# Kernel tuning notes

Measured on AMD Instinct MI355X. Metric: run time of the kernel, lower is better.

## Reference

```python
import jax, jax.numpy as jnp
import numpy as np

N, E = 50000, 800000
D_IN_N, D_IN_E, D_OUT = 64, 64, 64


def setup_inputs() -> dict:
    key = jax.random.key(0)
    ks = jax.random.split(key, 10)
    stdv = 1.0 / np.sqrt(D_OUT)
    u = lambda k, shape: jax.random.uniform(k, shape, jnp.float32, -stdv, stdv)
    return {
        "nf": jax.random.normal(ks[0], (N, D_IN_N), jnp.float32),
        "ef": jax.random.normal(ks[1], (E, D_IN_E), jnp.float32),
        "src": jax.random.randint(ks[2], (E,), 0, N, jnp.int32),
        "dst": jax.random.randint(ks[3], (E,), 0, N, jnp.int32),
        "W_node": u(ks[4], (D_IN_N, D_OUT)),
        "W_edge": u(ks[5], (D_IN_E, D_OUT)),
        "bias_node": u(ks[6], (D_OUT,)),
        "bias_edge": u(ks[7], (D_OUT,)),
        "W_dense": u(ks[8], (2 * D_OUT, D_OUT)),  # Linear(2*out, out) weight, stored transposed
        "b_dense": u(ks[9], (D_OUT,)),
    }


def reference(nf, ef, src, dst, W_node, W_edge, bias_node, bias_edge, W_dense, b_dense):
    n_nodes = nf.shape[0]
    # input projections
    nf_h = nf @ W_node                     # [N, D]
    ef_h = ef @ W_edge                     # [E, D]
    # update_all: mean of incoming edge features per dst node (0 for isolated nodes, DGL default)
    deg = jax.ops.segment_sum(jnp.ones((ef_h.shape[0],), ef_h.dtype), dst, num_segments=n_nodes)
    nb_ef = jax.ops.segment_sum(ef_h, dst, num_segments=n_nodes) / jnp.maximum(deg, 1.0)[:, None]
    # apply_nodes: nf = act(nf + bias)
    nf_out = jax.nn.relu(nf_h + bias_node)
    # apply_edges (uses updated nf): cat([ef + nb_ef[dst], (nf[src]+nf[dst])/2]) -> Linear -> +bias -> act
    tmp_ef = ef_h + nb_ef[dst]             # [E, D]
    srcdst_nf = (nf_out[src] + nf_out[dst]) * 0.5
    ef_out = jnp.concatenate([tmp_ef, srcdst_nf], axis=1) @ W_dense + b_dense + bias_edge
    ef_out = jax.nn.relu(ef_out)
    return nf_out, ef_out
```

## Files before the change

### kernel.cpp

```cpp
#include <hip/hip_runtime.h>

#define D 64

typedef __attribute__((ext_vector_type(8))) short short8;
typedef __attribute__((ext_vector_type(4))) float f32x4;

__device__ __forceinline__ ushort f2b(float f) {
    union { float f; unsigned u; } x; x.f = f;
    unsigned r = x.u + 0x7FFFu + ((x.u >> 16) & 1u);
    return (ushort)(r >> 16);
}
__device__ __forceinline__ float b2f(ushort u) {
    union { float f; unsigned u; } x; x.u = ((unsigned)u) << 16;
    return x.f;
}
__device__ __forceinline__ short8 pack8(float4 a, float4 b) {
    short8 r;
    r[0] = (short)f2b(a.x); r[1] = (short)f2b(a.y); r[2] = (short)f2b(a.z); r[3] = (short)f2b(a.w);
    r[4] = (short)f2b(b.x); r[5] = (short)f2b(b.y); r[6] = (short)f2b(b.z); r[7] = (short)f2b(b.w);
    return r;
}

#define LDA 72

__global__ __launch_bounds__(256) void fused_front_kernel(
    const float* __restrict__ nf, const float* __restrict__ Wn,
    const float* __restrict__ bias, const float* __restrict__ Wd,
    float* __restrict__ out, ushort* __restrict__ nfp_b, int N,
    const int* __restrict__ dst, int* __restrict__ deg_i, int E,
    const float* __restrict__ W_edge, const float* __restrict__ b_dense,
    const float* __restrict__ bias_edge, ushort* __restrict__ Wcomb_b,
    float* __restrict__ bias2, int NPB, int HB)
{
    __shared__ ushort Bn[64 * LDA];
    __shared__ ushort Bd[64 * LDA];
    __shared__ ushort Vs[64 * LDA];
    const int tid = threadIdx.x;
    const int bid = blockIdx.x;

    if (bid < NPB) {
        const long row0 = (long)bid * 64;
        const int w = tid >> 6, lane = tid & 63;
        const int lr = lane & 15, g = lane >> 4;
        const bool odd = lane & 1;

        {
            int k = tid >> 2, n0 = (tid & 3) * 16;
            const float4* wr = (const float4*)(Wn + (long)k * D + n0);
            float4 v0 = wr[0], v1 = wr[1], v2 = wr[2], v3 = wr[3];
            float vs[16] = {v0.x, v0.y, v0.z, v0.w, v1.x, v1.y, v1.z, v1.w,
                            v2.x, v2.y, v2.z, v2.w, v3.x, v3.y, v3.z, v3.w};
            #pragma unroll
            for (int j = 0; j < 16; ++j) Bn[(n0 + j) * LDA + k] = f2b(vs[j]);
            const float4* wd = (const float4*)(Wd + (long)(D + k) * D + n0);
            float4 u0 = wd[0], u1 = wd[1], u2 = wd[2], u3 = wd[3];
            float us[16] = {u0.x, u0.y, u0.z, u0.w, u1.x, u1.y, u1.z, u1.w,
                            u2.x, u2.y, u2.z, u2.w, u3.x, u3.y, u3.z, u3.w};
            #pragma unroll
            for (int j = 0; j < 16; ++j) Bd[(n0 + j) * LDA + k] = f2b(0.5f * us[j]);
        }

        long era = row0 + 16 * w + lr; if (era >= N) era = N - 1;
        const float4* ap = (const float4*)(nf + era * D);
        float4 v0 = ap[2 * g], v1 = ap[2 * g + 1];
        float4 v2 = ap[8 + 2 * g], v3 = ap[8 + 2 * g + 1];
        short8 a0 = pack8(v0, v1), a1 = pack8(v2, v3);
        __syncthreads();

        f32x4 acc[4];
        #pragma unroll
        for (int t = 0; t < 4; ++t) {
            f32x4 z = {0.f, 0.f, 0.f, 0.f};
            short8 b0 = *(const short8*)&Bn[(16 * t + lr) * LDA + 8 * g];
            short8 b1 = *(const short8*)&Bn[(16 * t + lr) * LDA + 32 + 8 * g];
            z = __builtin_amdgcn_mfma_f32_16x16x32_bf16(a0, b0, z, 0, 0, 0);
            z = __builtin_amdgcn_mfma_f32_16x16x32_bf16(a1, b1, z, 0, 0, 0);
            acc[t] = z;
        }
        #pragma unroll
        for (int t = 0; t < 4; ++t) {
            int c = 16 * t + lr;
            float bb = bias[c];
            #pragma unroll
            for (int reg = 0; reg < 4; ++reg) {
                int r = 16 * w + 4 * g + reg;
                float v = fmaxf(acc[t][reg] + bb, 0.f);
                long rg = row0 + r;
                if (rg < N) out[rg * D + c] = v;
                Vs[r * LDA + c] = f2b(v);
            }
        }
        __syncthreads();

        short8 c0 = *(const short8*)&Vs[(16 * w + lr) * LDA + 8 * g];
        short8 c1 = *(const short8*)&Vs[(16 * w + lr) * LDA + 32 + 8 * g];
        f32x4 acc2[4];
        #pragma unroll
        for (int t = 0; t < 4; ++t) {
            f32x4 z = {0.f, 0.f, 0.f, 0.f};
            short8 b0 = *(const short8*)&Bd[(16 * t + lr) * LDA + 8 * g];
            short8 b1 = *(const short8*)&Bd[(16 * t + lr) * LDA + 32 + 8 * g];
            z = __builtin_amdgcn_mfma_f32_16x16x32_bf16(c0, b0, z, 0, 0, 0);
            z = __builtin_amdgcn_mfma_f32_16x16x32_bf16(c1, b1, z, 0, 0, 0);
            acc2[t] = z;
        }
        const int rb = 16 * w + 4 * g + (odd ? 2 : 0);
        long e0 = row0 + rb, e1 = row0 + rb + 1;
        #pragma unroll
        for (int t = 0; t < 4; ++t) {
            float p0 = __shfl_xor(acc2[t][0], 1, 64);
            float p1 = __shfl_xor(acc2[t][1], 1, 64);
            float p2 = __shfl_xor(acc2[t][2], 1, 64);
            float p3 = __shfl_xor(acc2[t][3], 1, 64);
            float lo0, hi0, lo1, hi1;
            if (odd) { lo0 = p2; hi0 = acc2[t][2]; lo1 = p3; hi1 = acc2[t][3]; }
            else     { lo0 = acc2[t][0]; hi0 = p0; lo1 = acc2[t][1]; hi1 = p1; }
            int cbase = 16 * t + (lr & ~1);
            unsigned dw0 = ((unsigned)f2b(hi0) << 16) | (unsigned)f2b(lo0);
            unsigned dw1 = ((unsigned)f2b(hi1) << 16) | (unsigned)f2b(lo1);
            if (e0 < N) *(unsigned*)(nfp_b + e0 * D + cbase) = dw0;
            if (e1 < N) *(unsigned*)(nfp_b + e1 * D + cbase) = dw1;
        }
    } else if (bid < NPB + HB) {
        int i = (bid - NPB) * 256 + tid;
        if (i < E) atomicAdd(deg_i + dst[i], 1);
    } else {
        for (int idx = tid; idx < D * D; idx += 256) {
            int k = idx >> 6, n = idx & 63;
            float s = 0.f;
            #pragma unroll 8
            for (int j = 0; j < D; ++j)
                s = fmaf(W_edge[k * D + j], Wd[j * D + n], s);
            Wcomb_b[n * D + k] = f2b(s);
        }
        if (tid < D) bias2[tid] = b_dense[tid] + bias_edge[tid];
    }
}

__global__ __launch_bounds__(256) void scanA_kernel(
    const int* __restrict__ deg_i, int* __restrict__ pos,
    int* __restrict__ bsum, int N)
{
    __shared__ int s[256];
    const int tid = threadIdx.x;
    const int i = blockIdx.x * 256 + tid;
    int v = (i < N) ? deg_i[i] : 0;
    s[tid] = v;
    __syncthreads();
    #pragma unroll
    for (int off = 1; off < 256; off <<= 1) {
        int t = (tid >= off) ? s[tid - off] : 0;
        __syncthreads();
        s[tid] += t;
        __syncthreads();
    }
    if (i < N) pos[i] = s[tid] - v;
    if (tid == 255) bsum[blockIdx.x] = s[255];
}

__global__ __launch_bounds__(256) void scanB_kernel(int* __restrict__ bsum, int NB)
{
    __shared__ int s[256];
    const int tid = threadIdx.x;
    int v = (tid < NB) ? bsum[tid] : 0;
    s[tid] = v;
    __syncthreads();
    #pragma unroll
    for (int off = 1; off < 256; off <<= 1) {
        int t = (tid >= off) ? s[tid - off] : 0;
        __syncthreads();
        s[tid] += t;
        __syncthreads();
    }
    if (tid < NB) bsum[tid] = s[tid] - v;
}

__global__ __launch_bounds__(256) void scanC_kernel(
    const int* __restrict__ pos, int* __restrict__ cursor,
    const int* __restrict__ bsum, int N)
{
    int i = blockIdx.x * 256 + threadIdx.x;
    if (i < N) cursor[i] = pos[i] + bsum[blockIdx.x];
}

__global__ __launch_bounds__(256) void scatter_kernel(
    const int* __restrict__ dst, int* __restrict__ cursor,
    int2* __restrict__ sorted_ed, int E)
{
    int i = blockIdx.x * 256 + threadIdx.x;
    if (i < E) {
        int dv = dst[i];
        int slot = atomicAdd(cursor + dv, 1);
        sorted_ed[slot] = make_int2(i, dv);
    }
}

#define SEG_ROWS 256
#define SLSTR 34
__global__ __launch_bounds__(256) void efp_seg_kernel(
    const float* __restrict__ ef, const int2* __restrict__ sorted_ed,
    const ushort* __restrict__ Wt, ushort* __restrict__ efp,
    float* __restrict__ nb_sum, int E)
{
    __shared__ unsigned Slds[SEG_ROWS * SLSTR];
    __shared__ int dsts[SEG_ROWS];
    const int tid = threadIdx.x;
    const long s0 = (long)blockIdx.x * SEG_ROWS;

    const int w = tid >> 6, lane = tid & 63;
    const int lr = lane & 15, g = lane >> 4;
    const bool odd = lane & 1;

    long gde[4];
    #pragma unroll
    for (int tt = 0; tt < 4; ++tt) {
        long s = s0 + 64 * tt + 16 * w + lr;
        if (s >= E) s = E - 1;
        gde[tt] = (long)sorted_ed[s].x;
    }
    float4 va[4][4];
    #pragma unroll
    for (int tt = 0; tt < 4; ++tt) {
        const float4* ap = (const float4*)(ef + gde[tt] * D);
        va[tt][0] = ap[2 * g];     va[tt][1] = ap[2 * g + 1];
        va[tt][2] = ap[8 + 2 * g]; va[tt][3] = ap[8 + 2 * g + 1];
    }
    int rbl[4]; long seo[4][2];
    #pragma unroll
    for (int tt = 0; tt < 4; ++tt) {
        rbl[tt] = 64 * tt + 16 * w + 4 * g + (odd ? 2 : 0);
        long s = s0 + rbl[tt];
        if (s > E - 2) s = (E - 2) & ~1L;
        int4 q = *(const int4*)&sorted_ed[s];
        seo[tt][0] = (long)q.x * D;
        seo[tt][1] = (long)q.z * D;
    }
    {
        long s = s0 + tid;
        dsts[tid] = (s < E) ? sorted_ed[s].y : -1;
    }

    short8 bf0[4], bf1[4];
    #pragma unroll
    for (int t = 0; t < 4; ++t) {
        bf0[t] = *(const short8*)&Wt[(16 * t + lr) * D + 8 * g];
        bf1[t] = *(const short8*)&Wt[(16 * t + lr) * D + 32 + 8 * g];
    }

    #pragma unroll
    for (int tt = 0; tt < 4; ++tt) {
        short8 a0 = pack8(va[tt][0], va[tt][1]);
        short8 a1 = pack8(va[tt][2], va[tt][3]);
        f32x4 acc[4];
        #pragma unroll
        for (int t = 0; t < 4; ++t) {
            f32x4 z = {0.f, 0.f, 0.f, 0.f};
            z = __builtin_amdgcn_mfma_f32_16x16x32_bf16(a0, bf0[t], z, 0, 0, 0);
            z = __builtin_amdgcn_mfma_f32_16x16x32_bf16(a1, bf1[t], z, 0, 0, 0);
            acc[t] = z;
        }

        const int rb = rbl[tt];
        long sl0 = s0 + rb, sl1 = s0 + rb + 1;
        #pragma unroll
        for (int t = 0; t < 4; ++t) {
            float p0 = __shfl_xor(acc[t][0], 1, 64);
            float p1 = __shfl_xor(acc[t][1], 1, 64);
            float p2 = __shfl_xor(acc[t][2], 1, 64);
            float p3 = __shfl_xor(acc[t][3], 1, 64);
            float lo0, hi0, lo1, hi1;
            if (odd) { lo0 = p2; hi0 = acc[t][2]; lo1 = p3; hi1 = acc[t][3]; }
            else     { lo0 = acc[t][0]; hi0 = p0; lo1 = acc[t][1]; hi1 = p1; }
            int cbase = 16 * t + (lr & ~1);
            int dc = cbase >> 1;
            unsigned dw0 = ((unsigned)f2b(hi0) << 16) | (unsigned)f2b(lo0);
            unsigned dw1 = ((unsigned)f2b(hi1) << 16) | (unsigned)f2b(lo1);
            if (sl0 < E) *(unsigned*)(efp + seo[tt][0] + cbase) = dw0;
            if (sl1 < E) *(unsigned*)(efp + seo[tt][1] + cbase) = dw1;
            Slds[rb * SLSTR + dc]       = dw0;
            Slds[(rb + 1) * SLSTR + dc] = dw1;
        }
    }
    __syncthreads();

    {
        const int dwc = tid & 31;
        const int r0 = (tid >> 5) * 32;
        float seg0 = 0.f, seg1 = 0.f;
        int cur = dsts[r0];
        #pragma unroll 4
        for (int r = r0; r < r0 + 32; ++r) {
            int dv = dsts[r];
            unsigned u = Slds[r * SLSTR + dwc];
            if (dv != cur) {
                if (cur >= 0) {
                    atomicAdd(nb_sum + (long)cur * D + 2 * dwc, seg0);
                    atomicAdd(nb_sum + (long)cur * D + 2 * dwc + 1, seg1);
                }
                seg0 = seg1 = 0.f;
                cur = dv;
            }
            seg0 += b2f((ushort)(u & 0xffff));
            seg1 += b2f((ushort)(u >> 16));
        }
        if (cur >= 0) {
            atomicAdd(nb_sum + (long)cur * D + 2 * dwc, seg0);
            atomicAdd(nb_sum + (long)cur * D + 2 * dwc + 1, seg1);
        }
    }
}

__global__ __launch_bounds__(256) void ndp_lite_kernel(
    const float* __restrict__ nb_sum, const int* __restrict__ deg_i,
    const ushort* __restrict__ nfp_b, ushort* __restrict__ ndp_b, int N)
{
    long i = (long)blockIdx.x * 256 + threadIdx.x;
    long node = i >> 3;
    int cb = (int)(i & 7);
    if (node >= N) return;
    float inv = 1.0f / fmaxf((float)deg_i[node], 1.0f);
    const float4* sp = (const float4*)(nb_sum + node * D + cb * 8);
    float4 x0 = sp[0], x1 = sp[1];
    short8 np = *(const short8*)(nfp_b + node * D + cb * 8);
    short8 r;
    r[0] = (short)f2b(x0.x * inv + b2f((ushort)np[0]));
    r[1] = (short)f2b(x0.y * inv + b2f((ushort)np[1]));
    r[2] = (short)f2b(x0.z * inv + b2f((ushort)np[2]));
    r[3] = (short)f2b(x0.w * inv + b2f((ushort)np[3]));
    r[4] = (short)f2b(x1.x * inv + b2f((ushort)np[4]));
    r[5] = (short)f2b(x1.y * inv + b2f((ushort)np[5]));
    r[6] = (short)f2b(x1.z * inv + b2f((ushort)np[6]));
    r[7] = (short)f2b(x1.w * inv + b2f((ushort)np[7]));
    *(short8*)(ndp_b + node * D + cb * 8) = r;
}

__global__ __launch_bounds__(256) void final_kernel(
    const ushort* __restrict__ efp, const int* __restrict__ src,
    const int* __restrict__ dst, const ushort* __restrict__ ndp_b,
    const ushort* __restrict__ nfp_b, const float* __restrict__ bias2,
    float* __restrict__ out, int E)
{
    long idx = (long)blockIdx.x * 256 + threadIdx.x;
    long e = idx >> 2;
    int q = (int)(idx & 3);
    if (e >= E) return;
    int dv = dst[e], sv = src[e];
    const short8* ep = (const short8*)(efp + e * D + q * 16);
    const short8* np = (const short8*)(ndp_b + (long)dv * D + q * 16);
    const short8* sp = (const short8*)(nfp_b + (long)sv * D + q * 16);
    short8 e0 = ep[0], e1 = ep[1];
    short8 n0 = np[0], n1 = np[1];
    short8 s0 = sp[0], s1 = sp[1];
    const float4* bp = (const float4*)(bias2 + q * 16);
    float4 b0 = bp[0], b1 = bp[1], b2 = bp[2], b3 = bp[3];

    float r[16];
    #pragma unroll
    for (int j = 0; j < 8; ++j) {
        r[j]     = b2f((ushort)e0[j]) + b2f((ushort)n0[j]) + b2f((ushort)s0[j]);
        r[8 + j] = b2f((ushort)e1[j]) + b2f((ushort)n1[j]) + b2f((ushort)s1[j]);
    }
    float4* op = (float4*)(out + e * D + q * 16);
    op[0] = make_float4(fmaxf(r[0] + b0.x, 0.f), fmaxf(r[1] + b0.y, 0.f),
                        fmaxf(r[2] + b0.z, 0.f), fmaxf(r[3] + b0.w, 0.f));
    op[1] = make_float4(fmaxf(r[4] + b1.x, 0.f), fmaxf(r[5] + b1.y, 0.f),
                        fmaxf(r[6] + b1.z, 0.f), fmaxf(r[7] + b1.w, 0.f));
    op[2] = make_float4(fmaxf(r[8] + b2.x, 0.f), fmaxf(r[9] + b2.y, 0.f),
                        fmaxf(r[10] + b2.z, 0.f), fmaxf(r[11] + b2.w, 0.f));
    op[3] = make_float4(fmaxf(r[12] + b3.x, 0.f), fmaxf(r[13] + b3.y, 0.f),
                        fmaxf(r[14] + b3.z, 0.f), fmaxf(r[15] + b3.w, 0.f));
}

extern "C" void kernel_launch(void* const* d_in, const int* in_sizes, int n_in,
                              void* d_out, int out_size, void* d_ws, size_t ws_size,
                              hipStream_t stream) {
    const float* nf        = (const float*)d_in[0];
    const float* ef        = (const float*)d_in[1];
    const int*   src       = (const int*)d_in[2];
    const int*   dst       = (const int*)d_in[3];
    const float* W_node    = (const float*)d_in[4];
    const float* W_edge    = (const float*)d_in[5];
    const float* bias_node = (const float*)d_in[6];
    const float* bias_edge = (const float*)d_in[7];
    const float* W_dense   = (const float*)d_in[8];
    const float* b_dense   = (const float*)d_in[9];

    const int N = in_sizes[0] / D;
    const int E = in_sizes[1] / D;
    const int NB = (N + 255) / 256;
    const int NPB = (N + 63) / 64;
    const int HB = (E + 255) / 256;

    float* nf_out = (float*)d_out;
    float* ef_out = (float*)d_out + (size_t)N * D;

    char* p = (char*)d_ws;
    int*    deg_i    = (int*)p;     p += (size_t)N * 4;
    float*  nb_sum   = (float*)p;   p += (size_t)N * D * 4;
    size_t  zbytes   = (size_t)(p - (char*)d_ws);
    int*    pos      = (int*)p;     p += (size_t)N * 4;
    int*    cursor   = (int*)p;     p += (size_t)N * 4;
    int*    bsum     = (int*)p;     p += 256 * 4;
    int2*   sorted_ed= (int2*)p;    p += (size_t)E * 8;
    ushort* nfp_b    = (ushort*)p;  p += (size_t)N * D * 2;
    ushort* ndp_b    = (ushort*)p;  p += (size_t)N * D * 2;
    ushort* Wcomb_b  = (ushort*)p;  p += D * D * 2;
    float*  bias2    = (float*)p;   p += 256;
    ushort* efp      = (ushort*)p;

    hipMemsetAsync(d_ws, 0, zbytes, stream);

    fused_front_kernel<<<NPB + HB + 1, 256, 0, stream>>>(
        nf, W_node, bias_node, W_dense, nf_out, nfp_b, N,
        dst, deg_i, E, W_edge, b_dense, bias_edge, Wcomb_b, bias2, NPB, HB);
    scanA_kernel<<<NB, 256, 0, stream>>>(deg_i, pos, bsum, N);
    scanB_kernel<<<1, 256, 0, stream>>>(bsum, NB);
    scanC_kernel<<<NB, 256, 0, stream>>>(pos, cursor, bsum, N);
    scatter_kernel<<<(E + 255) / 256, 256, 0, stream>>>(dst, cursor, sorted_ed, E);
    efp_seg_kernel<<<(E + SEG_ROWS - 1) / SEG_ROWS, 256, 0, stream>>>(
        ef, sorted_ed, Wcomb_b, efp, nb_sum, E);
    ndp_lite_kernel<<<(int)(((size_t)N * 8 + 255) / 256), 256, 0, stream>>>(
        nb_sum, deg_i, nfp_b, ndp_b, N);
    final_kernel<<<(int)(((size_t)E * 4 + 255) / 256), 256, 0, stream>>>(
        efp, src, dst, ndp_b, nfp_b, bias2, ef_out, E);
}
```

Baseline: 358.4 us.

## Store projected edge features in dst-sorted order and iterate final pass over sorted edges

The scatter step now records src alongside edge id and dst in a 16-byte sorted record. The segment kernel writes the bf16 edge projections contiguously in sorted position instead of scattering them by original edge id. The final kernel walks edges in sorted order, reading efp contiguously and gathering dst-node rows with locality, then scatters its fp32 output rows back to the original edge positions. This trades coalesced efp writes and dst-local gathers for scattered output writes and a larger sorted index array.

```diff
diff --git a/kernel.cpp b/kernel.cpp
--- a/kernel.cpp
+++ b/kernel.cpp
@@ -184,21 +184,21 @@
 }
 
 __global__ __launch_bounds__(256) void scatter_kernel(
-    const int* __restrict__ dst, int* __restrict__ cursor,
-    int2* __restrict__ sorted_ed, int E)
+    const int* __restrict__ dst, const int* __restrict__ src,
+    int* __restrict__ cursor, int4* __restrict__ sorted_eds, int E)
 {
     int i = blockIdx.x * 256 + threadIdx.x;
     if (i < E) {
         int dv = dst[i];
         int slot = atomicAdd(cursor + dv, 1);
-        sorted_ed[slot] = make_int2(i, dv);
+        sorted_eds[slot] = make_int4(i, dv, src[i], 0);
     }
 }
 
 #define SEG_ROWS 256
 #define SLSTR 34
 __global__ __launch_bounds__(256) void efp_seg_kernel(
-    const float* __restrict__ ef, const int2* __restrict__ sorted_ed,
+    const float* __restrict__ ef, const int4* __restrict__ sorted_eds,
     const ushort* __restrict__ Wt, ushort* __restrict__ efp,
     float* __restrict__ nb_sum, int E)
 {
@@ -216,7 +216,7 @@
     for (int tt = 0; tt < 4; ++tt) {
         long s = s0 + 64 * tt + 16 * w + lr;
         if (s >= E) s = E - 1;
-        gde[tt] = (long)sorted_ed[s].x;
+        gde[tt] = (long)sorted_eds[s].x;
     }
     float4 va[4][4];
     #pragma unroll
@@ -225,19 +225,9 @@
         va[tt][0] = ap[2 * g];     va[tt][1] = ap[2 * g + 1];
         va[tt][2] = ap[8 + 2 * g]; va[tt][3] = ap[8 + 2 * g + 1];
     }
-    int rbl[4]; long seo[4][2];
-    #pragma unroll
-    for (int tt = 0; tt < 4; ++tt) {
-        rbl[tt] = 64 * tt + 16 * w + 4 * g + (odd ? 2 : 0);
-        long s = s0 + rbl[tt];
-        if (s > E - 2) s = (E - 2) & ~1L;
-        int4 q = *(const int4*)&sorted_ed[s];
-        seo[tt][0] = (long)q.x * D;
-        seo[tt][1] = (long)q.z * D;
-    }
     {
         long s = s0 + tid;
-        dsts[tid] = (s < E) ? sorted_ed[s].y : -1;
+        dsts[tid] = (s < E) ? sorted_eds[s].y : -1;
     }
 
     short8 bf0[4], bf1[4];
@@ -260,7 +250,7 @@
             acc[t] = z;
         }
 
-        const int rb = rbl[tt];
+        const int rb = 64 * tt + 16 * w + 4 * g + (odd ? 2 : 0);
         long sl0 = s0 + rb, sl1 = s0 + rb + 1;
         #pragma unroll
         for (int t = 0; t < 4; ++t) {
@@ -275,8 +265,8 @@
             int dc = cbase >> 1;
             unsigned dw0 = ((unsigned)f2b(hi0) << 16) | (unsigned)f2b(lo0);
             unsigned dw1 = ((unsigned)f2b(hi1) << 16) | (unsigned)f2b(lo1);
-            if (sl0 < E) *(unsigned*)(efp + seo[tt][0] + cbase) = dw0;
-            if (sl1 < E) *(unsigned*)(efp + seo[tt][1] + cbase) = dw1;
+            if (sl0 < E) *(unsigned*)(efp + sl0 * D + cbase) = dw0;
+            if (sl1 < E) *(unsigned*)(efp + sl1 * D + cbase) = dw1;
             Slds[rb * SLSTR + dc]       = dw0;
             Slds[(rb + 1) * SLSTR + dc] = dw1;
         }
@@ -335,17 +325,18 @@
 }
 
 __global__ __launch_bounds__(256) void final_kernel(
-    const ushort* __restrict__ efp, const int* __restrict__ src,
-    const int* __restrict__ dst, const ushort* __restrict__ ndp_b,
-    const ushort* __restrict__ nfp_b, const float* __restrict__ bias2,
-    float* __restrict__ out, int E)
+    const ushort* __restrict__ efp, const int4* __restrict__ sorted_eds,
+    const ushort* __restrict__ ndp_b, const ushort* __restrict__ nfp_b,
+    const float* __restrict__ bias2, float* __restrict__ out, int E)
 {
     long idx = (long)blockIdx.x * 256 + threadIdx.x;
-    long e = idx >> 2;
+    long s = idx >> 2;
     int q = (int)(idx & 3);
-    if (e >= E) return;
-    int dv = dst[e], sv = src[e];
-    const short8* ep = (const short8*)(efp + e * D + q * 16);
+    if (s >= E) return;
+    int4 ed = sorted_eds[s];
+    long eid = ed.x;
+    int dv = ed.y, sv = ed.z;
+    const short8* ep = (const short8*)(efp + s * D + q * 16);
     const short8* np = (const short8*)(ndp_b + (long)dv * D + q * 16);
     const short8* sp = (const short8*)(nfp_b + (long)sv * D + q * 16);
     short8 e0 = ep[0], e1 = ep[1];
@@ -360,7 +351,7 @@
         r[j]     = b2f((ushort)e0[j]) + b2f((ushort)n0[j]) + b2f((ushort)s0[j]);
         r[8 + j] = b2f((ushort)e1[j]) + b2f((ushort)n1[j]) + b2f((ushort)s1[j]);
     }
-    float4* op = (float4*)(out + e * D + q * 16);
+    float4* op = (float4*)(out + eid * D + q * 16);
     op[0] = make_float4(fmaxf(r[0] + b0.x, 0.f), fmaxf(r[1] + b0.y, 0.f),
                         fmaxf(r[2] + b0.z, 0.f), fmaxf(r[3] + b0.w, 0.f));
     op[1] = make_float4(fmaxf(r[4] + b1.x, 0.f), fmaxf(r[5] + b1.y, 0.f),
@@ -401,7 +392,7 @@
     int*    pos      = (int*)p;     p += (size_t)N * 4;
     int*    cursor   = (int*)p;     p += (size_t)N * 4;
     int*    bsum     = (int*)p;     p += 256 * 4;
-    int2*   sorted_ed= (int2*)p;    p += (size_t)E * 8;
+    int4*   sorted_eds=(int4*)p;    p += (size_t)E * 16;
     ushort* nfp_b    = (ushort*)p;  p += (size_t)N * D * 2;
     ushort* ndp_b    = (ushort*)p;  p += (size_t)N * D * 2;
     ushort* Wcomb_b  = (ushort*)p;  p += D * D * 2;
@@ -416,11 +407,11 @@
     scanA_kernel<<<NB, 256, 0, stream>>>(deg_i, pos, bsum, N);
     scanB_kernel<<<1, 256, 0, stream>>>(bsum, NB);
     scanC_kernel<<<NB, 256, 0, stream>>>(pos, cursor, bsum, N);
-    scatter_kernel<<<(E + 255) / 256, 256, 0, stream>>>(dst, cursor, sorted_ed, E);
+    scatter_kernel<<<(E + 255) / 256, 256, 0, stream>>>(dst, src, cursor, sorted_eds, E);
     efp_seg_kernel<<<(E + SEG_ROWS - 1) / SEG_ROWS, 256, 0, stream>>>(
-        ef, sorted_ed, Wcomb_b, efp, nb_sum, E);
+        ef, sorted_eds, Wcomb_b, efp, nb_sum, E);
     ndp_lite_kernel<<<(int)(((size_t)N * 8 + 255) / 256), 256, 0, stream>>>(
         nb_sum, deg_i, nfp_b, ndp_b, N);
     final_kernel<<<(int)(((size_t)E * 4 + 255) / 256), 256, 0, stream>>>(
-        efp, src, dst, ndp_b, nfp_b, bias2, ef_out, E);
-}
+        efp, sorted_eds, ndp_b, nfp_b, bias2, ef_out, E);
+}
```

Result: faster. 343.9 us (-4.1%).
